# Kernel optimization log

Measured on AMD Instinct MI355X. Metric: run time of the kernel, lower is better.

Reference implementation:

```python
import jax, jax.numpy as jnp
import numpy as np

NODES = 14      # input_size: nodes per graph
IN_F = 24       # seq_len: node feature dim
HID1 = 32
HID2 = 64       # hid_feats
HEADS = 2
OUT = 24        # output_size
B = 2048        # number of graphs
SLOPE = 0.2


def _make_edges():
    # fully connected (no self loops) within each 14-node graph
    pairs = np.array([(i, j) for i in range(NODES) for j in range(NODES) if i != j]).T  # [2,182]
    offs = (np.arange(B) * NODES)[:, None]
    src = (pairs[0][None, :] + offs).reshape(-1)
    dst = (pairs[1][None, :] + offs).reshape(-1)
    return np.stack([src, dst]).astype(np.int32)  # [2, 372736]


def setup_inputs() -> dict:
    key = jax.random.key(0)
    ks = jax.random.split(key, 16)
    N = B * NODES
    x = jax.random.normal(ks[0], (N, IN_F), dtype=jnp.float32)
    y = jax.random.normal(ks[1], (N, OUT), dtype=jnp.float32)
    edge_index = jnp.asarray(_make_edges())
    batch = jnp.repeat(jnp.arange(B, dtype=jnp.int32), NODES)
    s = 0.1
    params = dict(
        W1=jax.random.normal(ks[2], (IN_F, HEADS * HID1), dtype=jnp.float32) * s,
        a_src1=jax.random.normal(ks[3], (HEADS, HID1), dtype=jnp.float32) * s,
        a_dst1=jax.random.normal(ks[4], (HEADS, HID1), dtype=jnp.float32) * s,
        b1=jnp.zeros((HID1,), dtype=jnp.float32),
        W2=jax.random.normal(ks[5], (HID1, HEADS * HID2), dtype=jnp.float32) * s,
        a_src2=jax.random.normal(ks[6], (HEADS, HID2), dtype=jnp.float32) * s,
        a_dst2=jax.random.normal(ks[7], (HEADS, HID2), dtype=jnp.float32) * s,
        b2=jnp.zeros((HID2,), dtype=jnp.float32),
        Wf1=jax.random.normal(ks[8], (NODES, HID2, 8), dtype=jnp.float32) * s,
        bf1=jnp.zeros((NODES, 8), dtype=jnp.float32),
        Wf2=jax.random.normal(ks[9], (NODES, 8, OUT), dtype=jnp.float32) * s,
        bf2=jnp.zeros((NODES, OUT), dtype=jnp.float32),
    )
    return {"x": x, "y": y, "edge_index": edge_index, "batch": batch, **params}


def gat_conv(x, src, dst, W, a_src, a_dst, b):
    # PyG GATConv, concat=False (mean over heads), self-loops already in src/dst
    N = x.shape[0]
    H, F = a_src.shape
    xh = (x @ W).reshape(N, H, F)                       # [N,H,F]
    al_s = (xh * a_src).sum(-1)                         # [N,H]
    al_d = (xh * a_dst).sum(-1)                         # [N,H]
    alpha = jax.nn.leaky_relu(al_s[src] + al_d[dst], SLOPE)  # [E,H]
    amax = jax.ops.segment_max(alpha, dst, num_segments=N)
    ex = jnp.exp(alpha - amax[dst])
    den = jax.ops.segment_sum(ex, dst, num_segments=N)
    w = ex / den[dst]                                   # softmax per target node
    out = jax.ops.segment_sum(w[:, :, None] * xh[src], dst, num_segments=N)  # [N,H,F]
    return out.mean(axis=1) + b


def reference(x, y, edge_index, batch, W1, a_src1, a_dst1, b1, W2, a_src2, a_dst2, b2, Wf1, bf1, Wf2, bf2):
    N = x.shape[0]
    loops = jnp.arange(N, dtype=edge_index.dtype)
    src = jnp.concatenate([edge_index[0], loops])
    dst = jnp.concatenate([edge_index[1], loops])
    h = jax.nn.elu(gat_conv(x, src, dst, W1, a_src1, a_dst1, b1))   # [N,32]
    h = gat_conv(h, src, dst, W2, a_src2, a_dst2, b2)               # [N,64]
    # batch regroup: batch ids are contiguous per graph, so the Python
    # gather-loop in the original is exactly a reshape
    nb = N // NODES
    xg = h.reshape(nb, NODES, HID2).transpose(1, 0, 2)   # [14, B, 64]
    yg = y.reshape(nb, NODES, OUT)                       # [B, 14, out]
    # per-node-index MLP ensemble, batched over the 14 indices
    hh = jax.nn.relu(jnp.einsum('kbh,kho->kbo', xg, Wf1) + bf1[:, None, :])
    pred = jax.nn.sigmoid(jnp.einsum('kbo,kop->kbp', hh, Wf2) + bf2[:, None, :])  # [14,B,out]
    return pred, yg
```

## Files before the change

kernel.cpp:

```cpp
#include <hip/hip_runtime.h>

#define NODES 14
#define IN_F 24
#define HID1 32
#define HID2 64
#define OUT_F 24
#define SLOPE 0.2f

#define U_US1 0
#define U_UD1 48
#define U_US2 96
#define U_UD2 160

#define GPB 4
#define XS_S 28
#define H1_S 36
#define H2_S 68
#define WT_S 20
#define PHASE_FENCE() __builtin_amdgcn_sched_barrier(0)

__global__ __launch_bounds__(256) void compute_uvecs(
    const float* __restrict__ W1, const float* __restrict__ a_src1,
    const float* __restrict__ a_dst1,
    const float* __restrict__ W2, const float* __restrict__ a_src2,
    const float* __restrict__ a_dst2, float* __restrict__ u)
{
  const int tid = threadIdx.x;
  if (tid < 96) {
    const int sd = (tid >= 48), r = tid - sd * 48;
    const int h = (r >= IN_F), k = r - h * IN_F;
    const float* av = sd ? a_dst1 : a_src1;
    float s = 0.f;
#pragma unroll
    for (int f = 0; f < HID1; ++f)
      s += W1[k * 64 + h * HID1 + f] * av[h * HID1 + f];
    u[(sd ? U_UD1 : U_US1) + h * IN_F + k] = s;
  } else if (tid < 224) {
    const int j = tid - 96;
    const int sd = (j >= 64), r = j - sd * 64;
    const int h = (r >= HID1), k = r - h * HID1;
    const float* av = sd ? a_dst2 : a_src2;
    float s = 0.f;
#pragma unroll
    for (int f = 0; f < HID2; ++f)
      s += W2[k * 128 + h * HID2 + f] * av[h * HID2 + f];
    u[(sd ? U_UD2 : U_US2) + h * HID1 + k] = s;
  }
}

__global__ __launch_bounds__(64 * GPB) void gnn_fused(
    const float* __restrict__ x, const float* __restrict__ y,
    const float* __restrict__ W1, const float* __restrict__ b1,
    const float* __restrict__ W2, const float* __restrict__ b2,
    const float* __restrict__ Wf1, const float* __restrict__ bf1,
    const float* __restrict__ Wf2, const float* __restrict__ bf2,
    const float* __restrict__ uvec,
    float* __restrict__ out, int ngraphs)
{
  const int tid  = threadIdx.x;
  const int lane = tid & 63;
  const int wv   = tid >> 6;
  const int gu   = __builtin_amdgcn_readfirstlane(blockIdx.x * GPB + wv);
  if (gu >= ngraphs) return;

  __shared__ __align__(16) float xs[GPB][NODES * XS_S];
  __shared__ __align__(16) float h1s[GPB][NODES * H1_S];
  __shared__ __align__(16) float h2s[GPB][NODES * H2_S];
  __shared__ __align__(16) float wt[GPB][28 * WT_S];
  __shared__ __align__(16) float als[GPB][32];
  __shared__ __align__(16) float ald[GPB][32];
  __shared__ __align__(16) float hhs[GPB][120];

  const float* xg = x + (size_t)gu * (NODES * IN_F);

  float w1r[IN_F];
#pragma unroll
  for (int k = 0; k < IN_F; ++k) w1r[k] = W1[k * 64 + lane];
  float w2r[64];
#pragma unroll
  for (int k = 0; k < HID1; ++k) {
    w2r[k]      = W2[k * 128 + lane];
    w2r[32 + k] = W2[k * 128 + 64 + lane];
  }
  {
    const float4* x4 = (const float4*)xg;
#pragma unroll
    for (int i = lane; i < (NODES * IN_F) / 4; i += 64) {
      const float4 v = x4[i];
      const int n = (i * 4) / IN_F, k = (i * 4) - n * IN_F;
      *(float4*)&xs[wv][n * XS_S + k] = v;
    }
  }
  PHASE_FENCE();

  {
    const float4* y4 = (const float4*)(y + (size_t)gu * (NODES * OUT_F));
    float4* o4 = (float4*)(out + (size_t)NODES * ngraphs * OUT_F
                               + (size_t)gu * (NODES * OUT_F));
    for (int i = lane; i < (NODES * OUT_F) / 4; i += 64) o4[i] = y4[i];
  }

  float xcol[NODES];
#pragma unroll 2
  for (int n = 0; n < NODES; ++n) {
    float acc = 0.f;
#pragma unroll
    for (int k4 = 0; k4 < IN_F / 4; ++k4) {
      const float4 xv = *(const float4*)&xs[wv][n * XS_S + k4 * 4];
      acc += xv.x * w1r[k4 * 4 + 0] + xv.y * w1r[k4 * 4 + 1]
           + xv.z * w1r[k4 * 4 + 2] + xv.w * w1r[k4 * 4 + 3];
    }
    xcol[n] = acc;
  }

  if (lane < 56) {
    const int n = lane >> 2, h = (lane >> 1) & 1, sd = lane & 1;
    const float* uu = uvec + (sd ? U_UD1 : U_US1) + h * IN_F;
    float s = 0.f;
#pragma unroll
    for (int k4 = 0; k4 < 6; ++k4) {
      const float4 xv = *(const float4*)&xs[wv][n * XS_S + k4 * 4];
      const float4 uv = *(const float4*)&uu[k4 * 4];
      s += xv.x * uv.x + xv.y * uv.y + xv.z * uv.z + xv.w * uv.w;
    }
    (sd ? ald : als)[wv][h * 16 + n] = s;
  }
  if (lane < NODES * 2) {
    const int j = lane >> 1, h = lane & 1;
    const float ad = ald[wv][h * 16 + j];
    const float4 A0 = *(const float4*)&als[wv][h * 16 + 0];
    const float4 A1 = *(const float4*)&als[wv][h * 16 + 4];
    const float4 A2 = *(const float4*)&als[wv][h * 16 + 8];
    const float2 A3 = *(const float2*)&als[wv][h * 16 + 12];
    float a[NODES] = {A0.x, A0.y, A0.z, A0.w, A1.x, A1.y, A1.z, A1.w,
                      A2.x, A2.y, A2.z, A2.w, A3.x, A3.y};
    float m = -1e30f;
#pragma unroll
    for (int i = 0; i < NODES; ++i) {
      float v = a[i] + ad;
      v = v > 0.f ? v : SLOPE * v;
      a[i] = v; m = fmaxf(m, v);
    }
    float den = 0.f;
#pragma unroll
    for (int i = 0; i < NODES; ++i) { a[i] = __expf(a[i] - m); den += a[i]; }
    const float r = 1.f / den;
    float* wr = &wt[wv][(j * 2 + h) * WT_S];
    *(float4*)&wr[0]  = make_float4(a[0]*r,  a[1]*r,  a[2]*r,  a[3]*r);
    *(float4*)&wr[4]  = make_float4(a[4]*r,  a[5]*r,  a[6]*r,  a[7]*r);
    *(float4*)&wr[8]  = make_float4(a[8]*r,  a[9]*r,  a[10]*r, a[11]*r);
    *(float2*)&wr[12] = make_float2(a[12]*r, a[13]*r);
  }

  {
    const int h = lane >> 5, f5 = lane & 31;
    const float bb = b1[f5];
#pragma unroll 2
    for (int n = 0; n < NODES; ++n) {
      const float* wr = &wt[wv][(n * 2 + h) * WT_S];
      const float4 w0 = *(const float4*)&wr[0];
      const float4 w1 = *(const float4*)&wr[4];
      const float4 w2 = *(const float4*)&wr[8];
      const float2 w3 = *(const float2*)&wr[12];
      float o = w0.x*xcol[0] + w0.y*xcol[1] + w0.z*xcol[2] + w0.w*xcol[3]
              + w1.x*xcol[4] + w1.y*xcol[5] + w1.z*xcol[6] + w1.w*xcol[7]
              + w2.x*xcol[8] + w2.y*xcol[9] + w2.z*xcol[10] + w2.w*xcol[11]
              + w3.x*xcol[12] + w3.y*xcol[13];
      const float oo = __shfl_xor(o, 32);
      if (h == 0) {
        const float v = 0.5f * (o + oo) + bb;
        h1s[wv][n * H1_S + f5] = v > 0.f ? v : expm1f(v);
      }
    }
  }
  PHASE_FENCE();

  float acc0[NODES], acc1[NODES];
#pragma unroll 2
  for (int n = 0; n < NODES; ++n) {
    const float4 v0 = *(const float4*)&h1s[wv][n * H1_S + 0];
    const float4 v1 = *(const float4*)&h1s[wv][n * H1_S + 4];
    const float4 v2 = *(const float4*)&h1s[wv][n * H1_S + 8];
    const float4 v3 = *(const float4*)&h1s[wv][n * H1_S + 12];
    const float4 v4 = *(const float4*)&h1s[wv][n * H1_S + 16];
    const float4 v5 = *(const float4*)&h1s[wv][n * H1_S + 20];
    const float4 v6 = *(const float4*)&h1s[wv][n * H1_S + 24];
    const float4 v7 = *(const float4*)&h1s[wv][n * H1_S + 28];
    acc0[n] = v0.x*w2r[0] + v0.y*w2r[1] + v0.z*w2r[2] + v0.w*w2r[3]
            + v1.x*w2r[4] + v1.y*w2r[5] + v1.z*w2r[6] + v1.w*w2r[7]
            + v2.x*w2r[8] + v2.y*w2r[9] + v2.z*w2r[10] + v2.w*w2r[11]
            + v3.x*w2r[12] + v3.y*w2r[13] + v3.z*w2r[14] + v3.w*w2r[15]
            + v4.x*w2r[16] + v4.y*w2r[17] + v4.z*w2r[18] + v4.w*w2r[19]
            + v5.x*w2r[20] + v5.y*w2r[21] + v5.z*w2r[22] + v5.w*w2r[23]
            + v6.x*w2r[24] + v6.y*w2r[25] + v6.z*w2r[26] + v6.w*w2r[27]
            + v7.x*w2r[28] + v7.y*w2r[29] + v7.z*w2r[30] + v7.w*w2r[31];
    acc1[n] = v0.x*w2r[32] + v0.y*w2r[33] + v0.z*w2r[34] + v0.w*w2r[35]
            + v1.x*w2r[36] + v1.y*w2r[37] + v1.z*w2r[38] + v1.w*w2r[39]
            + v2.x*w2r[40] + v2.y*w2r[41] + v2.z*w2r[42] + v2.w*w2r[43]
            + v3.x*w2r[44] + v3.y*w2r[45] + v3.z*w2r[46] + v3.w*w2r[47]
            + v4.x*w2r[48] + v4.y*w2r[49] + v4.z*w2r[50] + v4.w*w2r[51]
            + v5.x*w2r[52] + v5.y*w2r[53] + v5.z*w2r[54] + v5.w*w2r[55]
            + v6.x*w2r[56] + v6.y*w2r[57] + v6.z*w2r[58] + v6.w*w2r[59]
            + v7.x*w2r[60] + v7.y*w2r[61] + v7.z*w2r[62] + v7.w*w2r[63];
  }

  if (lane < 56) {
    const int n = lane >> 2, h = (lane >> 1) & 1, sd = lane & 1;
    const float* uu = uvec + (sd ? U_UD2 : U_US2) + h * HID1;
    float s = 0.f;
#pragma unroll
    for (int k4 = 0; k4 < 8; ++k4) {
      const float4 hv = *(const float4*)&h1s[wv][n * H1_S + k4 * 4];
      const float4 uv = *(const float4*)&uu[k4 * 4];
      s += hv.x * uv.x + hv.y * uv.y + hv.z * uv.z + hv.w * uv.w;
    }
    (sd ? ald : als)[wv][h * 16 + n] = s;
  }
  if (lane < NODES * 2) {
    const int j = lane >> 1, h = lane & 1;
    const float ad = ald[wv][h * 16 + j];
    const float4 A0 = *(const float4*)&als[wv][h * 16 + 0];
    const float4 A1 = *(const float4*)&als[wv][h * 16 + 4];
    const float4 A2 = *(const float4*)&als[wv][h * 16 + 8];
    const float2 A3 = *(const float2*)&als[wv][h * 16 + 12];
    float a[NODES] = {A0.x, A0.y, A0.z, A0.w, A1.x, A1.y, A1.z, A1.w,
                      A2.x, A2.y, A2.z, A2.w, A3.x, A3.y};
    float m = -1e30f;
#pragma unroll
    for (int i = 0; i < NODES; ++i) {
      float v = a[i] + ad;
      v = v > 0.f ? v : SLOPE * v;
      a[i] = v; m = fmaxf(m, v);
    }
    float den = 0.f;
#pragma unroll
    for (int i = 0; i < NODES; ++i) { a[i] = __expf(a[i] - m); den += a[i]; }
    const float r = 1.f / den;
    float* wr = &wt[wv][(j * 2 + h) * WT_S];
    *(float4*)&wr[0]  = make_float4(a[0]*r,  a[1]*r,  a[2]*r,  a[3]*r);
    *(float4*)&wr[4]  = make_float4(a[4]*r,  a[5]*r,  a[6]*r,  a[7]*r);
    *(float4*)&wr[8]  = make_float4(a[8]*r,  a[9]*r,  a[10]*r, a[11]*r);
    *(float2*)&wr[12] = make_float2(a[12]*r, a[13]*r);
  }

  {
    const float bb = b2[lane];
#pragma unroll 2
    for (int n = 0; n < NODES; ++n) {
      const float* wr0 = &wt[wv][(n * 2 + 0) * WT_S];
      const float* wr1 = &wt[wv][(n * 2 + 1) * WT_S];
      const float4 p0 = *(const float4*)&wr0[0];
      const float4 p1 = *(const float4*)&wr0[4];
      const float4 p2 = *(const float4*)&wr0[8];
      const float2 p3 = *(const float2*)&wr0[12];
      const float4 q0 = *(const float4*)&wr1[0];
      const float4 q1 = *(const float4*)&wr1[4];
      const float4 q2 = *(const float4*)&wr1[8];
      const float2 q3 = *(const float2*)&wr1[12];
      const float o0 = p0.x*acc0[0] + p0.y*acc0[1] + p0.z*acc0[2] + p0.w*acc0[3]
                     + p1.x*acc0[4] + p1.y*acc0[5] + p1.z*acc0[6] + p1.w*acc0[7]
                     + p2.x*acc0[8] + p2.y*acc0[9] + p2.z*acc0[10] + p2.w*acc0[11]
                     + p3.x*acc0[12] + p3.y*acc0[13];
      const float o1 = q0.x*acc1[0] + q0.y*acc1[1] + q0.z*acc1[2] + q0.w*acc1[3]
                     + q1.x*acc1[4] + q1.y*acc1[5] + q1.z*acc1[6] + q1.w*acc1[7]
                     + q2.x*acc1[8] + q2.y*acc1[9] + q2.z*acc1[10] + q2.w*acc1[11]
                     + q3.x*acc1[12] + q3.y*acc1[13];
      h2s[wv][n * H2_S + lane] = 0.5f * (o0 + o1) + bb;
    }
  }
  PHASE_FENCE();

  if (lane < 56) {
    const int k = lane >> 2, e2 = (lane & 3) * 2;
    float a0 = bf1[k * 8 + e2], a1 = bf1[k * 8 + e2 + 1];
#pragma unroll
    for (int f4 = 0; f4 < 16; ++f4) {
      const float4 hv = *(const float4*)&h2s[wv][k * H2_S + f4 * 4];
      const float2 wa = *(const float2*)&Wf1[(k * HID2 + f4 * 4 + 0) * 8 + e2];
      const float2 wb = *(const float2*)&Wf1[(k * HID2 + f4 * 4 + 1) * 8 + e2];
      const float2 wc = *(const float2*)&Wf1[(k * HID2 + f4 * 4 + 2) * 8 + e2];
      const float2 wd = *(const float2*)&Wf1[(k * HID2 + f4 * 4 + 3) * 8 + e2];
      a0 += hv.x * wa.x + hv.y * wb.x + hv.z * wc.x + hv.w * wd.x;
      a1 += hv.x * wa.y + hv.y * wb.y + hv.z * wc.y + hv.w * wd.y;
    }
    *(float2*)&hhs[wv][k * 8 + e2] =
        make_float2(fmaxf(a0, 0.f), fmaxf(a1, 0.f));
  }

  for (int idx = lane; idx < NODES * (OUT_F / 4); idx += 64) {
    const int k = idx / (OUT_F / 4), o4 = (idx - k * (OUT_F / 4)) * 4;
    const float4 h0 = *(const float4*)&hhs[wv][k * 8];
    const float4 h1 = *(const float4*)&hhs[wv][k * 8 + 4];
    float4 acc = *(const float4*)&bf2[k * OUT_F + o4];
    const float he[8] = {h0.x, h0.y, h0.z, h0.w, h1.x, h1.y, h1.z, h1.w};
#pragma unroll
    for (int e = 0; e < 8; ++e) {
      const float4 wv4 = *(const float4*)&Wf2[(k * 8 + e) * OUT_F + o4];
      acc.x += he[e] * wv4.x; acc.y += he[e] * wv4.y;
      acc.z += he[e] * wv4.z; acc.w += he[e] * wv4.w;
    }
    acc.x = 1.f / (1.f + __expf(-acc.x));
    acc.y = 1.f / (1.f + __expf(-acc.y));
    acc.z = 1.f / (1.f + __expf(-acc.z));
    acc.w = 1.f / (1.f + __expf(-acc.w));
    *(float4*)&out[(size_t)k * ngraphs * OUT_F + (size_t)gu * OUT_F + o4] = acc;
  }
}

extern "C" void kernel_launch(void* const* d_in, const int* in_sizes, int n_in,
                              void* d_out, int out_size, void* d_ws, size_t ws_size,
                              hipStream_t stream) {
  const float* x      = (const float*)d_in[0];
  const float* y      = (const float*)d_in[1];
  const float* W1     = (const float*)d_in[4];
  const float* a_src1 = (const float*)d_in[5];
  const float* a_dst1 = (const float*)d_in[6];
  const float* b1     = (const float*)d_in[7];
  const float* W2     = (const float*)d_in[8];
  const float* a_src2 = (const float*)d_in[9];
  const float* a_dst2 = (const float*)d_in[10];
  const float* b2     = (const float*)d_in[11];
  const float* Wf1    = (const float*)d_in[12];
  const float* bf1    = (const float*)d_in[13];
  const float* Wf2    = (const float*)d_in[14];
  const float* bf2    = (const float*)d_in[15];
  float* out = (float*)d_out;
  float* u   = (float*)d_ws;

  const int nnodes  = in_sizes[0] / IN_F;
  const int ngraphs = nnodes / NODES;
  const int nblocks = (ngraphs + GPB - 1) / GPB;

  hipLaunchKernelGGL(compute_uvecs, dim3(1), dim3(256), 0, stream,
                     W1, a_src1, a_dst1, W2, a_src2, a_dst2, u);
  hipLaunchKernelGGL(gnn_fused, dim3(nblocks), dim3(64 * GPB), 0, stream,
                     x, y, W1, b1, W2, b2, Wf1, bf1, Wf2, bf2, u, out, ngraphs);
}
```

Baseline: 30.53 us.

## Split fused GNN kernel into four staged kernels with global intermediates

When the workspace is large enough, the single fused per-graph kernel is replaced by four kernels: GEMM1, layer-1 attention, GEMM2, and layer-2 attention plus MLP. Intermediates (xh1, h1, xh2) go to global workspace. The aim is to cut per-wave register pressure and raise occupancy by moving the weight-stationary GEMMs into their own kernels, each wave handling 7 nodes. In exchange it adds several MB of global traffic and three extra launches. The old fused kernel remains as a fallback.

```diff
diff --git a/kernel.cpp b/kernel.cpp
--- a/kernel.cpp
+++ b/kernel.cpp
@@ -12,11 +12,8 @@
 #define U_US2 96
 #define U_UD2 160
 
-#define GPB 4
-#define XS_S 28
-#define H1_S 36
-#define H2_S 68
 #define WT_S 20
+#define H2L_S 68
 #define PHASE_FENCE() __builtin_amdgcn_sched_barrier(0)
 
 __global__ __launch_bounds__(256) void compute_uvecs(
@@ -48,6 +45,301 @@
   }
 }
 
+
+__global__ __launch_bounds__(256) void k1_gemm1(
+    const float* __restrict__ x, const float* __restrict__ W1,
+    float* __restrict__ xh1, int nnodes)
+{
+  const int lane = threadIdx.x & 63;
+  const int wid = blockIdx.x * 4 + (threadIdx.x >> 6);
+  float w1r[IN_F];
+#pragma unroll
+  for (int k = 0; k < IN_F; ++k) w1r[k] = W1[k * 64 + lane];
+  const int n0 = wid * 7;
+#pragma unroll
+  for (int t = 0; t < 7; ++t) {
+    const int n = n0 + t;
+    if (n < nnodes) {
+      const float* xr = x + (size_t)n * IN_F;
+      float acc = 0.f;
+#pragma unroll
+      for (int k4 = 0; k4 < 6; ++k4) {
+        const float4 xv = *(const float4*)&xr[k4 * 4];
+        acc += xv.x * w1r[k4 * 4 + 0] + xv.y * w1r[k4 * 4 + 1]
+             + xv.z * w1r[k4 * 4 + 2] + xv.w * w1r[k4 * 4 + 3];
+      }
+      xh1[(size_t)n * 64 + lane] = acc;
+    }
+  }
+}
+
+__global__ __launch_bounds__(256) void k2_attn1(
+    const float* __restrict__ x, const float* __restrict__ xh1,
+    const float* __restrict__ uvec, const float* __restrict__ b1,
+    float* __restrict__ h1, int ngraphs)
+{
+  const int lane = threadIdx.x & 63;
+  const int wv = threadIdx.x >> 6;
+  const int gu = blockIdx.x * 4 + wv;
+  if (gu >= ngraphs) return;
+
+  __shared__ __align__(16) float wt[4][28 * WT_S];
+  __shared__ __align__(16) float als[4][32], ald[4][32];
+
+  const float* xg = x + (size_t)gu * (NODES * IN_F);
+
+  if (lane < 56) {
+    const int n = lane >> 2, h = (lane >> 1) & 1, sd = lane & 1;
+    const float* uu = uvec + (sd ? U_UD1 : U_US1) + h * IN_F;
+    float s = 0.f;
+#pragma unroll
+    for (int k4 = 0; k4 < 6; ++k4) {
+      const float4 xv = *(const float4*)&xg[n * IN_F + k4 * 4];
+      const float4 uv = *(const float4*)&uu[k4 * 4];
+      s += xv.x * uv.x + xv.y * uv.y + xv.z * uv.z + xv.w * uv.w;
+    }
+    (sd ? ald : als)[wv][h * 16 + n] = s;
+  }
+  if (lane < NODES * 2) {
+    const int j = lane >> 1, h = lane & 1;
+    const float ad = ald[wv][h * 16 + j];
+    const float4 A0 = *(const float4*)&als[wv][h * 16 + 0];
+    const float4 A1 = *(const float4*)&als[wv][h * 16 + 4];
+    const float4 A2 = *(const float4*)&als[wv][h * 16 + 8];
+    const float2 A3 = *(const float2*)&als[wv][h * 16 + 12];
+    float a[NODES] = {A0.x, A0.y, A0.z, A0.w, A1.x, A1.y, A1.z, A1.w,
+                      A2.x, A2.y, A2.z, A2.w, A3.x, A3.y};
+    float m = -1e30f;
+#pragma unroll
+    for (int i = 0; i < NODES; ++i) {
+      float v = a[i] + ad;
+      v = v > 0.f ? v : SLOPE * v;
+      a[i] = v; m = fmaxf(m, v);
+    }
+    float den = 0.f;
+#pragma unroll
+    for (int i = 0; i < NODES; ++i) { a[i] = __expf(a[i] - m); den += a[i]; }
+    const float r = 1.f / den;
+    float* wr = &wt[wv][(j * 2 + h) * WT_S];
+    *(float4*)&wr[0]  = make_float4(a[0]*r,  a[1]*r,  a[2]*r,  a[3]*r);
+    *(float4*)&wr[4]  = make_float4(a[4]*r,  a[5]*r,  a[6]*r,  a[7]*r);
+    *(float4*)&wr[8]  = make_float4(a[8]*r,  a[9]*r,  a[10]*r, a[11]*r);
+    *(float2*)&wr[12] = make_float2(a[12]*r, a[13]*r);
+  }
+  {
+    float xcol[NODES];
+    const float* xb = xh1 + (size_t)gu * (NODES * 64) + lane;
+#pragma unroll
+    for (int i = 0; i < NODES; ++i) xcol[i] = xb[i * 64];
+    const int h = lane >> 5, f5 = lane & 31;
+    const float bb = b1[f5];
+#pragma unroll 2
+    for (int n = 0; n < NODES; ++n) {
+      const float* wr = &wt[wv][(n * 2 + h) * WT_S];
+      const float4 w0 = *(const float4*)&wr[0];
+      const float4 w1 = *(const float4*)&wr[4];
+      const float4 w2 = *(const float4*)&wr[8];
+      const float2 w3 = *(const float2*)&wr[12];
+      float o = w0.x*xcol[0] + w0.y*xcol[1] + w0.z*xcol[2] + w0.w*xcol[3]
+              + w1.x*xcol[4] + w1.y*xcol[5] + w1.z*xcol[6] + w1.w*xcol[7]
+              + w2.x*xcol[8] + w2.y*xcol[9] + w2.z*xcol[10] + w2.w*xcol[11]
+              + w3.x*xcol[12] + w3.y*xcol[13];
+      const float oo = __shfl_xor(o, 32);
+      if (h == 0) {
+        const float v = 0.5f * (o + oo) + bb;
+        h1[((size_t)gu * NODES + n) * 32 + f5] = v > 0.f ? v : expm1f(v);
+      }
+    }
+  }
+}
+
+__global__ __launch_bounds__(256) void k3_gemm2(
+    const float* __restrict__ h1, const float* __restrict__ W2,
+    float* __restrict__ xh2, int nnodes)
+{
+  const int lane = threadIdx.x & 63;
+  const int wid = blockIdx.x * 4 + (threadIdx.x >> 6);
+  float w2r[64];
+#pragma unroll
+  for (int k = 0; k < HID1; ++k) {
+    w2r[k]      = W2[k * 128 + lane];
+    w2r[32 + k] = W2[k * 128 + 64 + lane];
+  }
+  const int n0 = wid * 7;
+#pragma unroll
+  for (int t = 0; t < 7; ++t) {
+    const int n = n0 + t;
+    if (n < nnodes) {
+      const float* hr = h1 + (size_t)n * 32;
+      const float4 v0 = *(const float4*)&hr[0];
+      const float4 v1 = *(const float4*)&hr[4];
+      const float4 v2 = *(const float4*)&hr[8];
+      const float4 v3 = *(const float4*)&hr[12];
+      const float4 v4 = *(const float4*)&hr[16];
+      const float4 v5 = *(const float4*)&hr[20];
+      const float4 v6 = *(const float4*)&hr[24];
+      const float4 v7 = *(const float4*)&hr[28];
+      const float a0 =
+          v0.x*w2r[0] + v0.y*w2r[1] + v0.z*w2r[2] + v0.w*w2r[3]
+        + v1.x*w2r[4] + v1.y*w2r[5] + v1.z*w2r[6] + v1.w*w2r[7]
+        + v2.x*w2r[8] + v2.y*w2r[9] + v2.z*w2r[10] + v2.w*w2r[11]
+        + v3.x*w2r[12] + v3.y*w2r[13] + v3.z*w2r[14] + v3.w*w2r[15]
+        + v4.x*w2r[16] + v4.y*w2r[17] + v4.z*w2r[18] + v4.w*w2r[19]
+        + v5.x*w2r[20] + v5.y*w2r[21] + v5.z*w2r[22] + v5.w*w2r[23]
+        + v6.x*w2r[24] + v6.y*w2r[25] + v6.z*w2r[26] + v6.w*w2r[27]
+        + v7.x*w2r[28] + v7.y*w2r[29] + v7.z*w2r[30] + v7.w*w2r[31];
+      const float a1 =
+          v0.x*w2r[32] + v0.y*w2r[33] + v0.z*w2r[34] + v0.w*w2r[35]
+        + v1.x*w2r[36] + v1.y*w2r[37] + v1.z*w2r[38] + v1.w*w2r[39]
+        + v2.x*w2r[40] + v2.y*w2r[41] + v2.z*w2r[42] + v2.w*w2r[43]
+        + v3.x*w2r[44] + v3.y*w2r[45] + v3.z*w2r[46] + v3.w*w2r[47]
+        + v4.x*w2r[48] + v4.y*w2r[49] + v4.z*w2r[50] + v4.w*w2r[51]
+        + v5.x*w2r[52] + v5.y*w2r[53] + v5.z*w2r[54] + v5.w*w2r[55]
+        + v6.x*w2r[56] + v6.y*w2r[57] + v6.z*w2r[58] + v6.w*w2r[59]
+        + v7.x*w2r[60] + v7.y*w2r[61] + v7.z*w2r[62] + v7.w*w2r[63];
+      xh2[(size_t)n * 128 + lane] = a0;
+      xh2[(size_t)n * 128 + 64 + lane] = a1;
+    }
+  }
+}
+
+__global__ __launch_bounds__(256) void k4_attn2_mlp(
+    const float* __restrict__ y, const float* __restrict__ h1,
+    const float* __restrict__ xh2, const float* __restrict__ uvec,
+    const float* __restrict__ b2,
+    const float* __restrict__ Wf1, const float* __restrict__ bf1,
+    const float* __restrict__ Wf2, const float* __restrict__ bf2,
+    float* __restrict__ out, int ngraphs)
+{
+  const int lane = threadIdx.x & 63;
+  const int wv = threadIdx.x >> 6;
+  const int gu = blockIdx.x * 4 + wv;
+  if (gu >= ngraphs) return;
+
+  __shared__ __align__(16) float wt[4][28 * WT_S];
+  __shared__ __align__(16) float als[4][32], ald[4][32];
+  __shared__ __align__(16) float h2s[4][NODES * H2L_S];
+  __shared__ __align__(16) float hhs[4][120];
+
+  {
+    const float4* y4 = (const float4*)(y + (size_t)gu * (NODES * OUT_F));
+    float4* o4 = (float4*)(out + (size_t)NODES * ngraphs * OUT_F
+                               + (size_t)gu * (NODES * OUT_F));
+    for (int i = lane; i < (NODES * OUT_F) / 4; i += 64) o4[i] = y4[i];
+  }
+
+  const float* hg = h1 + (size_t)gu * (NODES * 32);
+  if (lane < 56) {
+    const int n = lane >> 2, h = (lane >> 1) & 1, sd = lane & 1;
+    const float* uu = uvec + (sd ? U_UD2 : U_US2) + h * HID1;
+    float s = 0.f;
+#pragma unroll
+    for (int k4 = 0; k4 < 8; ++k4) {
+      const float4 hv = *(const float4*)&hg[n * 32 + k4 * 4];
+      const float4 uv = *(const float4*)&uu[k4 * 4];
+      s += hv.x * uv.x + hv.y * uv.y + hv.z * uv.z + hv.w * uv.w;
+    }
+    (sd ? ald : als)[wv][h * 16 + n] = s;
+  }
+  if (lane < NODES * 2) {
+    const int j = lane >> 1, h = lane & 1;
+    const float ad = ald[wv][h * 16 + j];
+    const float4 A0 = *(const float4*)&als[wv][h * 16 + 0];
+    const float4 A1 = *(const float4*)&als[wv][h * 16 + 4];
+    const float4 A2 = *(const float4*)&als[wv][h * 16 + 8];
+    const float2 A3 = *(const float2*)&als[wv][h * 16 + 12];
+    float a[NODES] = {A0.x, A0.y, A0.z, A0.w, A1.x, A1.y, A1.z, A1.w,
+                      A2.x, A2.y, A2.z, A2.w, A3.x, A3.y};
+    float m = -1e30f;
+#pragma unroll
+    for (int i = 0; i < NODES; ++i) {
+      float v = a[i] + ad;
+      v = v > 0.f ? v : SLOPE * v;
+      a[i] = v; m = fmaxf(m, v);
+    }
+    float den = 0.f;
+#pragma unroll
+    for (int i = 0; i < NODES; ++i) { a[i] = __expf(a[i] - m); den += a[i]; }
+    const float r = 1.f / den;
+    float* wr = &wt[wv][(j * 2 + h) * WT_S];
+    *(float4*)&wr[0]  = make_float4(a[0]*r,  a[1]*r,  a[2]*r,  a[3]*r);
+    *(float4*)&wr[4]  = make_float4(a[4]*r,  a[5]*r,  a[6]*r,  a[7]*r);
+    *(float4*)&wr[8]  = make_float4(a[8]*r,  a[9]*r,  a[10]*r, a[11]*r);
+    *(float2*)&wr[12] = make_float2(a[12]*r, a[13]*r);
+  }
+  {
+    float xc0[NODES], xc1[NODES];
+    const float* xb = xh2 + (size_t)gu * (NODES * 128);
+#pragma unroll
+    for (int i = 0; i < NODES; ++i) {
+      xc0[i] = xb[i * 128 + lane];
+      xc1[i] = xb[i * 128 + 64 + lane];
+    }
+    const float bb = b2[lane];
+#pragma unroll 2
+    for (int n = 0; n < NODES; ++n) {
+      const float* wr0 = &wt[wv][(n * 2 + 0) * WT_S];
+      const float* wr1 = &wt[wv][(n * 2 + 1) * WT_S];
+      const float4 p0 = *(const float4*)&wr0[0];
+      const float4 p1 = *(const float4*)&wr0[4];
+      const float4 p2 = *(const float4*)&wr0[8];
+      const float2 p3 = *(const float2*)&wr0[12];
+      const float4 q0 = *(const float4*)&wr1[0];
+      const float4 q1 = *(const float4*)&wr1[4];
+      const float4 q2 = *(const float4*)&wr1[8];
+      const float2 q3 = *(const float2*)&wr1[12];
+      const float o0 = p0.x*xc0[0] + p0.y*xc0[1] + p0.z*xc0[2] + p0.w*xc0[3]
+                     + p1.x*xc0[4] + p1.y*xc0[5] + p1.z*xc0[6] + p1.w*xc0[7]
+                     + p2.x*xc0[8] + p2.y*xc0[9] + p2.z*xc0[10] + p2.w*xc0[11]
+                     + p3.x*xc0[12] + p3.y*xc0[13];
+      const float o1 = q0.x*xc1[0] + q0.y*xc1[1] + q0.z*xc1[2] + q0.w*xc1[3]
+                     + q1.x*xc1[4] + q1.y*xc1[5] + q1.z*xc1[6] + q1.w*xc1[7]
+                     + q2.x*xc1[8] + q2.y*xc1[9] + q2.z*xc1[10] + q2.w*xc1[11]
+                     + q3.x*xc1[12] + q3.y*xc1[13];
+      h2s[wv][n * H2L_S + lane] = 0.5f * (o0 + o1) + bb;
+    }
+  }
+  PHASE_FENCE();
+  if (lane < 56) {
+    const int k = lane >> 2, e2 = (lane & 3) * 2;
+    float a0 = bf1[k * 8 + e2], a1 = bf1[k * 8 + e2 + 1];
+#pragma unroll
+    for (int f4 = 0; f4 < 16; ++f4) {
+      const float4 hv = *(const float4*)&h2s[wv][k * H2L_S + f4 * 4];
+      const float2 wa = *(const float2*)&Wf1[(k * HID2 + f4 * 4 + 0) * 8 + e2];
+      const float2 wb = *(const float2*)&Wf1[(k * HID2 + f4 * 4 + 1) * 8 + e2];
+      const float2 wc = *(const float2*)&Wf1[(k * HID2 + f4 * 4 + 2) * 8 + e2];
+      const float2 wd = *(const float2*)&Wf1[(k * HID2 + f4 * 4 + 3) * 8 + e2];
+      a0 += hv.x * wa.x + hv.y * wb.x + hv.z * wc.x + hv.w * wd.x;
+      a1 += hv.x * wa.y + hv.y * wb.y + hv.z * wc.y + hv.w * wd.y;
+    }
+    *(float2*)&hhs[wv][k * 8 + e2] =
+        make_float2(fmaxf(a0, 0.f), fmaxf(a1, 0.f));
+  }
+  for (int idx = lane; idx < NODES * (OUT_F / 4); idx += 64) {
+    const int k = idx / (OUT_F / 4), o4 = (idx - k * (OUT_F / 4)) * 4;
+    const float4 h0 = *(const float4*)&hhs[wv][k * 8];
+    const float4 hq = *(const float4*)&hhs[wv][k * 8 + 4];
+    float4 acc = *(const float4*)&bf2[k * OUT_F + o4];
+    const float he[8] = {h0.x, h0.y, h0.z, h0.w, hq.x, hq.y, hq.z, hq.w};
+#pragma unroll
+    for (int e = 0; e < 8; ++e) {
+      const float4 wv4 = *(const float4*)&Wf2[(k * 8 + e) * OUT_F + o4];
+      acc.x += he[e] * wv4.x; acc.y += he[e] * wv4.y;
+      acc.z += he[e] * wv4.z; acc.w += he[e] * wv4.w;
+    }
+    acc.x = 1.f / (1.f + __expf(-acc.x));
+    acc.y = 1.f / (1.f + __expf(-acc.y));
+    acc.z = 1.f / (1.f + __expf(-acc.z));
+    acc.w = 1.f / (1.f + __expf(-acc.w));
+    *(float4*)&out[(size_t)k * ngraphs * OUT_F + (size_t)gu * OUT_F + o4] = acc;
+  }
+}
+
+#define GPB 4
+#define XS_S 28
+#define H1_S 36
+#define H2_S 68
 __global__ __launch_bounds__(64 * GPB) void gnn_fused(
     const float* __restrict__ x, const float* __restrict__ y,
     const float* __restrict__ W1, const float* __restrict__ b1,
@@ -92,14 +384,12 @@
     }
   }
   PHASE_FENCE();
-
   {
     const float4* y4 = (const float4*)(y + (size_t)gu * (NODES * OUT_F));
     float4* o4 = (float4*)(out + (size_t)NODES * ngraphs * OUT_F
                                + (size_t)gu * (NODES * OUT_F));
     for (int i = lane; i < (NODES * OUT_F) / 4; i += 64) o4[i] = y4[i];
   }
-
   float xcol[NODES];
 #pragma unroll 2
   for (int n = 0; n < NODES; ++n) {
@@ -112,7 +402,6 @@
     }
     xcol[n] = acc;
   }
-
   if (lane < 56) {
     const int n = lane >> 2, h = (lane >> 1) & 1, sd = lane & 1;
     const float* uu = uvec + (sd ? U_UD1 : U_US1) + h * IN_F;
@@ -151,7 +440,6 @@
     *(float4*)&wr[8]  = make_float4(a[8]*r,  a[9]*r,  a[10]*r, a[11]*r);
     *(float2*)&wr[12] = make_float2(a[12]*r, a[13]*r);
   }
-
   {
     const int h = lane >> 5, f5 = lane & 31;
     const float bb = b1[f5];
@@ -174,7 +462,6 @@
     }
   }
   PHASE_FENCE();
-
   float acc0[NODES], acc1[NODES];
 #pragma unroll 2
   for (int n = 0; n < NODES; ++n) {
@@ -203,7 +490,6 @@
             + v6.x*w2r[56] + v6.y*w2r[57] + v6.z*w2r[58] + v6.w*w2r[59]
             + v7.x*w2r[60] + v7.y*w2r[61] + v7.z*w2r[62] + v7.w*w2r[63];
   }
-
   if (lane < 56) {
     const int n = lane >> 2, h = (lane >> 1) & 1, sd = lane & 1;
     const float* uu = uvec + (sd ? U_UD2 : U_US2) + h * HID1;
@@ -242,7 +528,6 @@
     *(float4*)&wr[8]  = make_float4(a[8]*r,  a[9]*r,  a[10]*r, a[11]*r);
     *(float2*)&wr[12] = make_float2(a[12]*r, a[13]*r);
   }
-
   {
     const float bb = b2[lane];
 #pragma unroll 2
@@ -269,7 +554,6 @@
     }
   }
   PHASE_FENCE();
-
   if (lane < 56) {
     const int k = lane >> 2, e2 = (lane & 3) * 2;
     float a0 = bf1[k * 8 + e2], a1 = bf1[k * 8 + e2 + 1];
@@ -286,13 +570,12 @@
     *(float2*)&hhs[wv][k * 8 + e2] =
         make_float2(fmaxf(a0, 0.f), fmaxf(a1, 0.f));
   }
-
   for (int idx = lane; idx < NODES * (OUT_F / 4); idx += 64) {
     const int k = idx / (OUT_F / 4), o4 = (idx - k * (OUT_F / 4)) * 4;
     const float4 h0 = *(const float4*)&hhs[wv][k * 8];
-    const float4 h1 = *(const float4*)&hhs[wv][k * 8 + 4];
+    const float4 hq = *(const float4*)&hhs[wv][k * 8 + 4];
     float4 acc = *(const float4*)&bf2[k * OUT_F + o4];
-    const float he[8] = {h0.x, h0.y, h0.z, h0.w, h1.x, h1.y, h1.z, h1.w};
+    const float he[8] = {h0.x, h0.y, h0.z, h0.w, hq.x, hq.y, hq.z, hq.w};
 #pragma unroll
     for (int e = 0; e < 8; ++e) {
       const float4 wv4 = *(const float4*)&Wf2[(k * 8 + e) * OUT_F + o4];
@@ -325,14 +608,35 @@
   const float* Wf2    = (const float*)d_in[14];
   const float* bf2    = (const float*)d_in[15];
   float* out = (float*)d_out;
-  float* u   = (float*)d_ws;
+  float* ws  = (float*)d_ws;
 
   const int nnodes  = in_sizes[0] / IN_F;
   const int ngraphs = nnodes / NODES;
-  const int nblocks = (ngraphs + GPB - 1) / GPB;
-
+
+  const size_t need = (256 + (size_t)nnodes * 224) * sizeof(float);
+
+  float* u = ws;
   hipLaunchKernelGGL(compute_uvecs, dim3(1), dim3(256), 0, stream,
                      W1, a_src1, a_dst1, W2, a_src2, a_dst2, u);
-  hipLaunchKernelGGL(gnn_fused, dim3(nblocks), dim3(64 * GPB), 0, stream,
-                     x, y, W1, b1, W2, b2, Wf1, bf1, Wf2, bf2, u, out, ngraphs);
+
+  if (ws_size >= need) {
+    float* xh1 = ws + 256;
+    float* h1  = xh1 + (size_t)nnodes * 64;
+    float* xh2 = h1  + (size_t)nnodes * 32;
+    const int nwaves = (nnodes + 6) / 7;
+    const int gblk   = (nwaves + 3) / 4;
+    const int ablk   = (ngraphs + 3) / 4;
+    hipLaunchKernelGGL(k1_gemm1, dim3(gblk), dim3(256), 0, stream,
+                       x, W1, xh1, nnodes);
+    hipLaunchKernelGGL(k2_attn1, dim3(ablk), dim3(256), 0, stream,
+                       x, xh1, u, b1, h1, ngraphs);
+    hipLaunchKernelGGL(k3_gemm2, dim3(gblk), dim3(256), 0, stream,
+                       h1, W2, xh2, nnodes);
+    hipLaunchKernelGGL(k4_attn2_mlp, dim3(ablk), dim3(256), 0, stream,
+                       y, h1, xh2, u, b2, Wf1, bf1, Wf2, bf2, out, ngraphs);
+  } else {
+    const int nblocks = (ngraphs + GPB - 1) / GPB;
+    hipLaunchKernelGGL(gnn_fused, dim3(nblocks), dim3(64 * GPB), 0, stream,
+                       x, y, W1, b1, W2, b2, Wf1, bf1, Wf2, bf2, u, out, ngraphs);
+  }
 }
```

Measured after the change: 53.34 us. 1.75x slower.

## Replace LDS staging with direct global reads and cross-lane readlane broadcasts

Applied to the files above, without the earlier changes.

Drops the shared-memory staging of node features x and reads them directly from global memory, relying on cache broadcast. The layer-2 input projection now broadcasts each hidden-1 value across lanes with readlane instead of vector LDS loads. The layer-2 attention weights stay in registers and are fetched with readlane rather than going through an LDS round trip. This cuts LDS traffic and LDS waits, but adds many scalar readlane instructions and uncoalesced per-lane global loads, and it raises register pressure.

```diff
diff --git a/kernel.cpp b/kernel.cpp
--- a/kernel.cpp
+++ b/kernel.cpp
@@ -13,11 +13,14 @@
 #define U_UD2 160
 
 #define GPB 4
-#define XS_S 28
 #define H1_S 36
 #define H2_S 68
 #define WT_S 20
 #define PHASE_FENCE() __builtin_amdgcn_sched_barrier(0)
+
+__device__ __forceinline__ float rdlane(float v, int l) {
+  return __int_as_float(__builtin_amdgcn_readlane(__float_as_int(v), l));
+}
 
 __global__ __launch_bounds__(256) void compute_uvecs(
     const float* __restrict__ W1, const float* __restrict__ a_src1,
@@ -63,10 +66,9 @@
   const int gu   = __builtin_amdgcn_readfirstlane(blockIdx.x * GPB + wv);
   if (gu >= ngraphs) return;
 
-  __shared__ __align__(16) float xs[GPB][NODES * XS_S];
   __shared__ __align__(16) float h1s[GPB][NODES * H1_S];
+  __shared__ __align__(16) float wt1[GPB][28 * WT_S];
   __shared__ __align__(16) float h2s[GPB][NODES * H2_S];
-  __shared__ __align__(16) float wt[GPB][28 * WT_S];
   __shared__ __align__(16) float als[GPB][32];
   __shared__ __align__(16) float ald[GPB][32];
   __shared__ __align__(16) float hhs[GPB][120];
@@ -81,15 +83,6 @@
   for (int k = 0; k < HID1; ++k) {
     w2r[k]      = W2[k * 128 + lane];
     w2r[32 + k] = W2[k * 128 + 64 + lane];
-  }
-  {
-    const float4* x4 = (const float4*)xg;
-#pragma unroll
-    for (int i = lane; i < (NODES * IN_F) / 4; i += 64) {
-      const float4 v = x4[i];
-      const int n = (i * 4) / IN_F, k = (i * 4) - n * IN_F;
-      *(float4*)&xs[wv][n * XS_S + k] = v;
-    }
   }
   PHASE_FENCE();
 
@@ -105,11 +98,7 @@
   for (int n = 0; n < NODES; ++n) {
     float acc = 0.f;
 #pragma unroll
-    for (int k4 = 0; k4 < IN_F / 4; ++k4) {
-      const float4 xv = *(const float4*)&xs[wv][n * XS_S + k4 * 4];
-      acc += xv.x * w1r[k4 * 4 + 0] + xv.y * w1r[k4 * 4 + 1]
-           + xv.z * w1r[k4 * 4 + 2] + xv.w * w1r[k4 * 4 + 3];
-    }
+    for (int k = 0; k < IN_F; ++k) acc += xg[n * IN_F + k] * w1r[k];
     xcol[n] = acc;
   }
 
@@ -119,7 +108,7 @@
     float s = 0.f;
 #pragma unroll
     for (int k4 = 0; k4 < 6; ++k4) {
-      const float4 xv = *(const float4*)&xs[wv][n * XS_S + k4 * 4];
+      const float4 xv = *(const float4*)&xg[n * IN_F + k4 * 4];
       const float4 uv = *(const float4*)&uu[k4 * 4];
       s += xv.x * uv.x + xv.y * uv.y + xv.z * uv.z + xv.w * uv.w;
     }
@@ -145,19 +134,20 @@
 #pragma unroll
     for (int i = 0; i < NODES; ++i) { a[i] = __expf(a[i] - m); den += a[i]; }
     const float r = 1.f / den;
-    float* wr = &wt[wv][(j * 2 + h) * WT_S];
+    float* wr = &wt1[wv][(j * 2 + h) * WT_S];
     *(float4*)&wr[0]  = make_float4(a[0]*r,  a[1]*r,  a[2]*r,  a[3]*r);
     *(float4*)&wr[4]  = make_float4(a[4]*r,  a[5]*r,  a[6]*r,  a[7]*r);
     *(float4*)&wr[8]  = make_float4(a[8]*r,  a[9]*r,  a[10]*r, a[11]*r);
     *(float2*)&wr[12] = make_float2(a[12]*r, a[13]*r);
   }
 
+  float h1r[NODES];
   {
     const int h = lane >> 5, f5 = lane & 31;
     const float bb = b1[f5];
 #pragma unroll 2
     for (int n = 0; n < NODES; ++n) {
-      const float* wr = &wt[wv][(n * 2 + h) * WT_S];
+      const float* wr = &wt1[wv][(n * 2 + h) * WT_S];
       const float4 w0 = *(const float4*)&wr[0];
       const float4 w1 = *(const float4*)&wr[4];
       const float4 w2 = *(const float4*)&wr[8];
@@ -167,10 +157,9 @@
               + w2.x*xcol[8] + w2.y*xcol[9] + w2.z*xcol[10] + w2.w*xcol[11]
               + w3.x*xcol[12] + w3.y*xcol[13];
       const float oo = __shfl_xor(o, 32);
-      if (h == 0) {
-        const float v = 0.5f * (o + oo) + bb;
-        h1s[wv][n * H1_S + f5] = v > 0.f ? v : expm1f(v);
-      }
+      const float v = 0.5f * (o + oo) + bb;
+      h1r[n] = v > 0.f ? v : expm1f(v);
+      if (lane < 32) h1s[wv][n * H1_S + lane] = h1r[n];
     }
   }
   PHASE_FENCE();
@@ -178,30 +167,14 @@
   float acc0[NODES], acc1[NODES];
 #pragma unroll 2
   for (int n = 0; n < NODES; ++n) {
-    const float4 v0 = *(const float4*)&h1s[wv][n * H1_S + 0];
-    const float4 v1 = *(const float4*)&h1s[wv][n * H1_S + 4];
-    const float4 v2 = *(const float4*)&h1s[wv][n * H1_S + 8];
-    const float4 v3 = *(const float4*)&h1s[wv][n * H1_S + 12];
-    const float4 v4 = *(const float4*)&h1s[wv][n * H1_S + 16];
-    const float4 v5 = *(const float4*)&h1s[wv][n * H1_S + 20];
-    const float4 v6 = *(const float4*)&h1s[wv][n * H1_S + 24];
-    const float4 v7 = *(const float4*)&h1s[wv][n * H1_S + 28];
-    acc0[n] = v0.x*w2r[0] + v0.y*w2r[1] + v0.z*w2r[2] + v0.w*w2r[3]
-            + v1.x*w2r[4] + v1.y*w2r[5] + v1.z*w2r[6] + v1.w*w2r[7]
-            + v2.x*w2r[8] + v2.y*w2r[9] + v2.z*w2r[10] + v2.w*w2r[11]
-            + v3.x*w2r[12] + v3.y*w2r[13] + v3.z*w2r[14] + v3.w*w2r[15]
-            + v4.x*w2r[16] + v4.y*w2r[17] + v4.z*w2r[18] + v4.w*w2r[19]
-            + v5.x*w2r[20] + v5.y*w2r[21] + v5.z*w2r[22] + v5.w*w2r[23]
-            + v6.x*w2r[24] + v6.y*w2r[25] + v6.z*w2r[26] + v6.w*w2r[27]
-            + v7.x*w2r[28] + v7.y*w2r[29] + v7.z*w2r[30] + v7.w*w2r[31];
-    acc1[n] = v0.x*w2r[32] + v0.y*w2r[33] + v0.z*w2r[34] + v0.w*w2r[35]
-            + v1.x*w2r[36] + v1.y*w2r[37] + v1.z*w2r[38] + v1.w*w2r[39]
-            + v2.x*w2r[40] + v2.y*w2r[41] + v2.z*w2r[42] + v2.w*w2r[43]
-            + v3.x*w2r[44] + v3.y*w2r[45] + v3.z*w2r[46] + v3.w*w2r[47]
-            + v4.x*w2r[48] + v4.y*w2r[49] + v4.z*w2r[50] + v4.w*w2r[51]
-            + v5.x*w2r[52] + v5.y*w2r[53] + v5.z*w2r[54] + v5.w*w2r[55]
-            + v6.x*w2r[56] + v6.y*w2r[57] + v6.z*w2r[58] + v6.w*w2r[59]
-            + v7.x*w2r[60] + v7.y*w2r[61] + v7.z*w2r[62] + v7.w*w2r[63];
+    float a0 = 0.f, a1 = 0.f;
+#pragma unroll
+    for (int k = 0; k < HID1; ++k) {
+      const float s = rdlane(h1r[n], k);
+      a0 += s * w2r[k];
+      a1 += s * w2r[32 + k];
+    }
+    acc0[n] = a0; acc1[n] = a1;
   }
 
   if (lane < 56) {
@@ -216,15 +189,25 @@
     }
     (sd ? ald : als)[wv][h * 16 + n] = s;
   }
-  if (lane < NODES * 2) {
+  float wt2reg[NODES];
+  {
     const int j = lane >> 1, h = lane & 1;
-    const float ad = ald[wv][h * 16 + j];
-    const float4 A0 = *(const float4*)&als[wv][h * 16 + 0];
-    const float4 A1 = *(const float4*)&als[wv][h * 16 + 4];
-    const float4 A2 = *(const float4*)&als[wv][h * 16 + 8];
-    const float2 A3 = *(const float2*)&als[wv][h * 16 + 12];
-    float a[NODES] = {A0.x, A0.y, A0.z, A0.w, A1.x, A1.y, A1.z, A1.w,
-                      A2.x, A2.y, A2.z, A2.w, A3.x, A3.y};
+    const bool act = lane < NODES * 2;
+    const float ad = act ? ald[wv][h * 16 + j] : 0.f;
+    float a[NODES];
+    if (act) {
+      const float4 A0 = *(const float4*)&als[wv][h * 16 + 0];
+      const float4 A1 = *(const float4*)&als[wv][h * 16 + 4];
+      const float4 A2 = *(const float4*)&als[wv][h * 16 + 8];
+      const float2 A3 = *(const float2*)&als[wv][h * 16 + 12];
+      a[0]=A0.x; a[1]=A0.y; a[2]=A0.z; a[3]=A0.w;
+      a[4]=A1.x; a[5]=A1.y; a[6]=A1.z; a[7]=A1.w;
+      a[8]=A2.x; a[9]=A2.y; a[10]=A2.z; a[11]=A2.w;
+      a[12]=A3.x; a[13]=A3.y;
+    } else {
+#pragma unroll
+      for (int i = 0; i < NODES; ++i) a[i] = 0.f;
+    }
     float m = -1e30f;
 #pragma unroll
     for (int i = 0; i < NODES; ++i) {
@@ -236,35 +219,21 @@
 #pragma unroll
     for (int i = 0; i < NODES; ++i) { a[i] = __expf(a[i] - m); den += a[i]; }
     const float r = 1.f / den;
-    float* wr = &wt[wv][(j * 2 + h) * WT_S];
-    *(float4*)&wr[0]  = make_float4(a[0]*r,  a[1]*r,  a[2]*r,  a[3]*r);
-    *(float4*)&wr[4]  = make_float4(a[4]*r,  a[5]*r,  a[6]*r,  a[7]*r);
-    *(float4*)&wr[8]  = make_float4(a[8]*r,  a[9]*r,  a[10]*r, a[11]*r);
-    *(float2*)&wr[12] = make_float2(a[12]*r, a[13]*r);
-  }
+#pragma unroll
+    for (int i = 0; i < NODES; ++i) wt2reg[i] = a[i] * r;
+  }
+  PHASE_FENCE();
 
   {
     const float bb = b2[lane];
 #pragma unroll 2
     for (int n = 0; n < NODES; ++n) {
-      const float* wr0 = &wt[wv][(n * 2 + 0) * WT_S];
-      const float* wr1 = &wt[wv][(n * 2 + 1) * WT_S];
-      const float4 p0 = *(const float4*)&wr0[0];
-      const float4 p1 = *(const float4*)&wr0[4];
-      const float4 p2 = *(const float4*)&wr0[8];
-      const float2 p3 = *(const float2*)&wr0[12];
-      const float4 q0 = *(const float4*)&wr1[0];
-      const float4 q1 = *(const float4*)&wr1[4];
-      const float4 q2 = *(const float4*)&wr1[8];
-      const float2 q3 = *(const float2*)&wr1[12];
-      const float o0 = p0.x*acc0[0] + p0.y*acc0[1] + p0.z*acc0[2] + p0.w*acc0[3]
-                     + p1.x*acc0[4] + p1.y*acc0[5] + p1.z*acc0[6] + p1.w*acc0[7]
-                     + p2.x*acc0[8] + p2.y*acc0[9] + p2.z*acc0[10] + p2.w*acc0[11]
-                     + p3.x*acc0[12] + p3.y*acc0[13];
-      const float o1 = q0.x*acc1[0] + q0.y*acc1[1] + q0.z*acc1[2] + q0.w*acc1[3]
-                     + q1.x*acc1[4] + q1.y*acc1[5] + q1.z*acc1[6] + q1.w*acc1[7]
-                     + q2.x*acc1[8] + q2.y*acc1[9] + q2.z*acc1[10] + q2.w*acc1[11]
-                     + q3.x*acc1[12] + q3.y*acc1[13];
+      float o0 = 0.f, o1 = 0.f;
+#pragma unroll
+      for (int i = 0; i < NODES; ++i) {
+        o0 += rdlane(wt2reg[i], 2 * n)     * acc0[i];
+        o1 += rdlane(wt2reg[i], 2 * n + 1) * acc1[i];
+      }
       h2s[wv][n * H2_S + lane] = 0.5f * (o0 + o1) + bb;
     }
   }
@@ -290,9 +259,9 @@
   for (int idx = lane; idx < NODES * (OUT_F / 4); idx += 64) {
     const int k = idx / (OUT_F / 4), o4 = (idx - k * (OUT_F / 4)) * 4;
     const float4 h0 = *(const float4*)&hhs[wv][k * 8];
-    const float4 h1 = *(const float4*)&hhs[wv][k * 8 + 4];
+    const float4 hq = *(const float4*)&hhs[wv][k * 8 + 4];
     float4 acc = *(const float4*)&bf2[k * OUT_F + o4];
-    const float he[8] = {h0.x, h0.y, h0.z, h0.w, h1.x, h1.y, h1.z, h1.w};
+    const float he[8] = {h0.x, h0.y, h0.z, h0.w, hq.x, hq.y, hq.z, hq.w};
 #pragma unroll
     for (int e = 0; e < 8; ++e) {
       const float4 wv4 = *(const float4*)&Wf2[(k * 8 + e) * OUT_F + o4];
```

Result: slower. 35.14 us (+15.1%).
